# Kernel optimization log

Measured on AMD Instinct MI355X. Metric: run time of the kernel, lower is better.

Reference implementation:

```python
import jax, jax.numpy as jnp
import numpy as np

N_NODES = 50000
N_EDGES = 800000
NODE_DIM = 128
EDGE_DIM = 16
OUT_DIM = 64
HEADS = 4


def setup_inputs() -> dict:
    key = jax.random.key(0)
    ks = jax.random.split(key, 12)
    x = jax.random.normal(ks[0], (N_NODES, NODE_DIM), jnp.float32)
    edge_index = jax.random.randint(ks[1], (2, N_EDGES), 0, N_NODES)
    batch = jnp.zeros((N_NODES,), jnp.int32)
    edge_attr = jax.random.normal(ks[2], (N_EDGES, EDGE_DIM), jnp.float32)
    s = 1.0 / np.sqrt(NODE_DIM)
    W = jax.random.normal(ks[3], (NODE_DIM, HEADS * OUT_DIM), jnp.float32) * s
    att_src = jax.random.normal(ks[4], (HEADS, OUT_DIM), jnp.float32) * 0.1
    att_dst = jax.random.normal(ks[5], (HEADS, OUT_DIM), jnp.float32) * 0.1
    W_e = jax.random.normal(ks[6], (EDGE_DIM, HEADS * OUT_DIM), jnp.float32) * (1.0 / np.sqrt(EDGE_DIM))
    att_edge = jax.random.normal(ks[7], (HEADS, OUT_DIM), jnp.float32) * 0.1
    bias = jnp.zeros((OUT_DIM,), jnp.float32)
    gamma = jnp.ones((OUT_DIM,), jnp.float32)
    beta = jnp.zeros((OUT_DIM,), jnp.float32)
    return {"x": x, "edge_index": edge_index, "batch": batch, "edge_attr": edge_attr,
            "W": W, "att_src": att_src, "att_dst": att_dst, "W_e": W_e,
            "att_edge": att_edge, "bias": bias, "gamma": gamma, "beta": beta}


def reference(x, edge_index, batch, edge_attr, W, att_src, att_dst, W_e, att_edge, bias, gamma, beta):
    N = x.shape[0]
    H, C = att_src.shape
    src, dst = edge_index[0], edge_index[1]
    E = src.shape[0]

    # add self loops; self-loop edge_attr = per-node mean of incoming edge attrs (PyG fill_value='mean')
    cnt = jax.ops.segment_sum(jnp.ones((E, 1), x.dtype), dst, num_segments=N)
    loop_attr = jax.ops.segment_sum(edge_attr, dst, num_segments=N) / jnp.maximum(cnt, 1.0)
    loop_idx = jnp.arange(N, dtype=src.dtype)
    src_f = jnp.concatenate([src, loop_idx])
    dst_f = jnp.concatenate([dst, loop_idx])
    ea = jnp.concatenate([edge_attr, loop_attr], axis=0)

    h = (x @ W).reshape(N, H, C)                       # [N,H,C]
    a_src = jnp.einsum('nhc,hc->nh', h, att_src)       # [N,H]
    a_dst = jnp.einsum('nhc,hc->nh', h, att_dst)
    e_emb = (ea @ W_e).reshape(-1, H, C)               # [E',H,C]
    a_edge = jnp.einsum('ehc,hc->eh', e_emb, att_edge)

    alpha = jax.nn.leaky_relu(a_src[src_f] + a_dst[dst_f] + a_edge, 0.2)  # [E',H]
    amax = jax.ops.segment_max(alpha, dst_f, num_segments=N)
    expa = jnp.exp(alpha - amax[dst_f])
    denom = jax.ops.segment_sum(expa, dst_f, num_segments=N)
    att = expa / (denom[dst_f] + 1e-16)                # segment softmax over dst

    msg = h[src_f] * att[:, :, None]                   # [E',H,C]
    out = jax.ops.segment_sum(msg, dst_f, num_segments=N)  # [N,H,C]
    out = out.mean(axis=1) + bias                      # concat=False -> head mean

    mu = out.mean(-1, keepdims=True)
    var = out.var(-1, keepdims=True)
    out = (out - mu) / jnp.sqrt(var + 1e-5) * gamma + beta
    return jax.nn.elu(out)
```

## Files before the change

kernel.cpp:

```cpp
#include <hip/hip_runtime.h>

typedef unsigned int u32;
typedef unsigned short u16;

static constexpr int NN  = 50000;
static constexpr int EE  = 800000;
static constexpr int CAP = 64;

typedef __attribute__((ext_vector_type(8))) short bf16x8;
typedef __attribute__((ext_vector_type(4))) float f32x4;
typedef __attribute__((ext_vector_type(4))) u32   u32x4;

__device__ inline float u2f(u32 u){ union{u32 i; float f;} v; v.i=u; return v.f; }
__device__ inline float bf2f(u16 u){ return u2f(((u32)u)<<16); }
__device__ inline u16 f2bf(float f){ union{float f; u32 i;} v; v.f=f; u32 i=v.i;
    return (u16)((i + 0x7fffu + ((i>>16)&1u))>>16); }
__device__ inline u32 pk2(float a, float b){ return (u32)f2bf(a) | ((u32)f2bf(b)<<16); }
__device__ inline float lrelu(float x){ return x > 0.f ? x : 0.2f*x; }

__device__ inline u32 pkh(float a, float b){
    union{ _Float16 h[2]; u32 u; } v;
    v.h[0] = (_Float16)a; v.h[1] = (_Float16)b;
    return v.u;
}
__device__ inline float hlo(u32 u){ union{u32 u; _Float16 h[2];} v; v.u=u; return (float)v.h[0]; }
__device__ inline float hhi(u32 u){ union{u32 u; _Float16 h[2];} v; v.u=u; return (float)v.h[1]; }

__device__ inline float ld(const void* base, size_t i, int f32m){
    return f32m ? ((const float*)base)[i] : bf2f(((const u16*)base)[i]);
}

__device__ inline float wsum(float v){
    #pragma unroll
    for (int m=1;m<64;m<<=1) v += __shfl_xor(v, m, 64);
    return v;
}

#if defined(__has_builtin)
#if __has_builtin(__builtin_amdgcn_fdot2_f32_bf16)
#define HAS_DOT2 1
#endif
#endif

#ifdef HAS_DOT2
typedef __attribute__((ext_vector_type(2))) __bf16 bf16x2;
#endif

__device__ inline float dot2acc(u32 hv, u32 wv, float acc){
#ifdef HAS_DOT2
    union { u32 u; bf16x2 v; } a, b; a.u = hv; b.u = wv;
    return __builtin_amdgcn_fdot2_f32_bf16(a.v, b.v, acc, false);
#else
    acc = fmaf(u2f(hv<<16),         u2f(wv<<16),         acc);
    acc = fmaf(u2f(hv&0xffff0000u), u2f(wv&0xffff0000u), acc);
    return acc;
#endif
}

__device__ inline int detect_f32(const u16* xraw){
    int lane = threadIdx.x & 63;
    bool bad = false;
    #pragma unroll
    for (int i = 0; i < 8; ++i){
        float v = bf2f(xraw[2*(lane + i*64)]);
        if (!(fabsf(v) < 1e10f)) bad = true;
    }
    return __any(bad) ? 1 : 0;
}

__device__ inline void edge_logits(const void* ea, int e, int f32m,
                                   const float* Ml, float* A){
    float v[16];
    if (f32m){
        const f32x4* r = ((const f32x4*)ea) + (size_t)e*4;
        f32x4 a = __builtin_nontemporal_load(r);
        f32x4 b = __builtin_nontemporal_load(r+1);
        f32x4 c = __builtin_nontemporal_load(r+2);
        f32x4 d = __builtin_nontemporal_load(r+3);
        v[0]=a[0]; v[1]=a[1]; v[2]=a[2]; v[3]=a[3];
        v[4]=b[0]; v[5]=b[1]; v[6]=b[2]; v[7]=b[3];
        v[8]=c[0]; v[9]=c[1]; v[10]=c[2]; v[11]=c[3];
        v[12]=d[0]; v[13]=d[1]; v[14]=d[2]; v[15]=d[3];
    } else {
        const u32x4* r = ((const u32x4*)ea) + (size_t)e*2;
        u32x4 q0 = __builtin_nontemporal_load(r);
        u32x4 q1 = __builtin_nontemporal_load(r+1);
        v[0]=u2f(q0[0]<<16); v[1]=u2f(q0[0]&0xffff0000u);
        v[2]=u2f(q0[1]<<16); v[3]=u2f(q0[1]&0xffff0000u);
        v[4]=u2f(q0[2]<<16); v[5]=u2f(q0[2]&0xffff0000u);
        v[6]=u2f(q0[3]<<16); v[7]=u2f(q0[3]&0xffff0000u);
        v[8]=u2f(q1[0]<<16); v[9]=u2f(q1[0]&0xffff0000u);
        v[10]=u2f(q1[1]<<16); v[11]=u2f(q1[1]&0xffff0000u);
        v[12]=u2f(q1[2]<<16); v[13]=u2f(q1[2]&0xffff0000u);
        v[14]=u2f(q1[3]<<16); v[15]=u2f(q1[3]&0xffff0000u);
    }
    float a0=0,a1=0,a2=0,a3=0;
    #pragma unroll
    for (int j = 0; j < 16; ++j){
        a0 = fmaf(v[j], Ml[j*4+0], a0);
        a1 = fmaf(v[j], Ml[j*4+1], a1);
        a2 = fmaf(v[j], Ml[j*4+2], a2);
        a3 = fmaf(v[j], Ml[j*4+3], a3);
    }
    A[0]=a0; A[1]=a1; A[2]=a2; A[3]=a3;
}

__global__ __launch_bounds__(256) void k_prep(const u16* __restrict__ xraw,
                                              const void* __restrict__ W,
                                              const void* __restrict__ att_src,
                                              const void* __restrict__ att_dst,
                                              const void* __restrict__ W_e,
                                              const void* __restrict__ att_edge,
                                              int* __restrict__ flag,
                                              u16* __restrict__ Wt,
                                              float* __restrict__ Mv){
    int f32m = detect_f32(xraw);
    int b = blockIdx.x, t = threadIdx.x;
    if (b == 0){
        if (t == 0) *flag = f32m;
        if (t < 64){
            int d = t >> 2, h = t & 3;
            float s = 0.f;
            for (int c = 0; c < 64; ++c)
                s += ld(W_e, d*256 + h*64 + c, f32m) * ld(att_edge, h*64 + c, f32m);
            Mv[t] = s;
        }
    } else if (b <= 128){
        int i = (b-1)*256 + t;
        int k = i >> 8, n = i & 255;
        Wt[n*128 + k] = f2bf(ld(W, (size_t)k*256 + n, f32m));
    } else {
        int i = (b-129)*256 + t;
        int c = i >> 7, k = i & 127;
        float s = 0.f;
        if (c < 8){
            int h = c & 3;
            const void* att = (c < 4) ? att_src : att_dst;
            for (int j = 0; j < 64; ++j)
                s += ld(W, (size_t)k*256 + h*64 + j, f32m) * ld(att, h*64 + j, f32m);
        }
        Wt[(size_t)(256 + c)*128 + k] = f2bf(s);
    }
}

static constexpr int LDSROW = 136;
static constexpr int CROW   = 264;

__global__ __launch_bounds__(256) void k_gemm(const void* __restrict__ x,
                                              const u16* __restrict__ Wt,
                                              const int* __restrict__ flag,
                                              u16* __restrict__ hbuf,
                                              float* __restrict__ a_src,
                                              float* __restrict__ a_dst, int N){
    __shared__ u16 sh[64*CROW];
    int f32m = *flag;
    int t = threadIdx.x;
    int row0 = blockIdx.x*64;
    if (f32m){
        const f32x4* xg = (const f32x4*)x;
        #pragma unroll
        for (int j=0;j<8;++j){
            int idx = t + j*256;
            int r = idx >> 5, c4 = idx & 31;
            int gr = row0 + r; if (gr >= N) gr = N-1;
            f32x4 v = __builtin_nontemporal_load(&xg[(size_t)gr*32 + c4]);
            *(uint2*)&sh[r*LDSROW + c4*4] = make_uint2(pk2(v[0],v[1]), pk2(v[2],v[3]));
        }
    } else {
        const u32x4* xg = (const u32x4*)x;
        #pragma unroll
        for (int j=0;j<4;++j){
            int idx = t + j*256;
            int r = idx >> 4, c8 = idx & 15;
            int gr = row0 + r; if (gr >= N) gr = N-1;
            u32x4 v = __builtin_nontemporal_load(&xg[(size_t)gr*16 + c8]);
            *(u32x4*)&sh[r*LDSROW + c8*8] = v;
        }
    }
    __syncthreads();
    int wave = t >> 6, lane = t & 63;
    int l15 = lane & 15, quad = lane >> 4;
    int mrow = wave*16 + l15;
    bf16x8 afr[4];
    #pragma unroll
    for (int s=0;s<4;++s)
        afr[s] = *(const bf16x8*)&sh[mrow*LDSROW + s*32 + quad*8];
    __syncthreads();
    f32x4 acc[17];
    #pragma unroll
    for (int tl=0;tl<17;++tl){
        f32x4 a = {0.f,0.f,0.f,0.f};
        #pragma unroll
        for (int s=0;s<4;++s){
            bf16x8 bfr = *(const bf16x8*)&Wt[(size_t)(tl*16 + l15)*128 + s*32 + quad*8];
            a = __builtin_amdgcn_mfma_f32_16x16x32_bf16(afr[s], bfr, a, 0, 0, 0);
        }
        acc[tl] = a;
    }
    int rbase = row0 + wave*16 + quad*4;
    #pragma unroll
    for (int r=0;r<4;++r){
        int gr = rbase + r;
        if (gr < N){
            if (l15 < 4)      a_src[gr*4 + l15]     = acc[16][r];
            else if (l15 < 8) a_dst[gr*4 + (l15-4)] = acc[16][r];
        }
    }
    #pragma unroll
    for (int r=0;r<4;++r){
        int row = wave*16 + quad*4 + r;
        #pragma unroll
        for (int tl=0;tl<4;++tl){
            u32 lo = pk2(acc[tl  ][r], acc[tl+4 ][r]);
            u32 hi = pk2(acc[tl+8][r], acc[tl+12][r]);
            *(uint2*)&sh[row*CROW + (tl*16 + l15)*4] = make_uint2(lo, hi);
        }
    }
    __syncthreads();
    uint4* h4 = (uint4*)hbuf;
    #pragma unroll
    for (int j=0;j<8;++j){
        int idx = t + j*256;
        int row = idx >> 5, c16 = idx & 31;
        if (row0 + row < N){
            uint4 v = *(const uint4*)&sh[row*CROW + c16*8];
            h4[(size_t)(row0 + row)*32 + c16] = v;
        }
    }
}

__global__ __launch_bounds__(256) void k_edge(const int* __restrict__ ei,
                                              const void* __restrict__ ea,
                                              const float* __restrict__ Mv,
                                              const int* __restrict__ flag,
                                              int* __restrict__ deg,
                                              u32* __restrict__ brec, int E){
    __shared__ float Ml[64];
    if (threadIdx.x < 64) Ml[threadIdx.x] = Mv[threadIdx.x];
    __syncthreads();
    int f32m = *flag;
    int base = blockIdx.x*512 + threadIdx.x;
    #pragma unroll
    for (int j=0;j<2;++j){
        int e = base + j*256;
        if (e >= E) continue;
        int src = __builtin_nontemporal_load(&ei[e]);
        int dst = __builtin_nontemporal_load(&ei[E + e]);
        float A[4];
        edge_logits(ea, e, f32m, Ml, A);
        int slot = atomicAdd(&deg[dst], 1);
        if (slot < CAP){
            size_t i3 = ((size_t)dst*CAP + slot)*3;
            brec[i3]   = (u32)src;
            brec[i3+1] = pkh(A[0], A[1]);
            brec[i3+2] = pkh(A[2], A[3]);
        }
    }
}

__global__ __launch_bounds__(256) void k_node(const int* __restrict__ deg,
                                              const u32* __restrict__ brec,
                                              const float* __restrict__ a_src,
                                              const float* __restrict__ a_dst,
                                              const u16* __restrict__ hbuf,
                                              const void* __restrict__ bias,
                                              const void* __restrict__ gamma,
                                              const void* __restrict__ beta,
                                              const int* __restrict__ flag,
                                              void* __restrict__ out, int N){
    __shared__ uint4 lrec[4][CAP+4];
    int f32m = *flag;
    int lane = threadIdx.x & 63;
    int slot = threadIdx.x >> 6;
    int n = blockIdx.x*4 + slot;
    int dg = deg[n];
    int dc = dg < CAP ? dg : CAP;
    float4 an  = ((const float4*)a_src)[n];
    float4 adn = ((const float4*)a_dst)[n];
    bool v0 = lane < dc;
    u32 src = (u32)n;
    float w0=0.f,w1=0.f,w2=0.f,w3=0.f;
    float a0=0.f,a1=0.f,a2=0.f,a3=0.f;
    if (v0){
        const u32* rp = brec + ((size_t)n*CAP + lane)*3;
        u32 s   = rp[0];
        u32 p01 = rp[1];
        u32 p23 = rp[2];
        src = s;
        a0 = hlo(p01); a1 = hhi(p01); a2 = hlo(p23); a3 = hhi(p23);
        float4 asg = ((const float4*)a_src)[s];
        w0 = expf(lrelu(asg.x + adn.x + a0));
        w1 = expf(lrelu(asg.y + adn.y + a1));
        w2 = expf(lrelu(asg.z + adn.z + a2));
        w3 = expf(lrelu(asg.w + adn.w + a3));
    }
    float dn0 = wsum(w0), dn1 = wsum(w1), dn2 = wsum(w2), dn3 = wsum(w3);
    float invd = 1.f / (float)(dg > 1 ? dg : 1);
    float ge0 = wsum(a0)*invd, ge1 = wsum(a1)*invd;
    float ge2 = wsum(a2)*invd, ge3 = wsum(a3)*invd;
    float exS0 = expf(lrelu(an.x + adn.x + ge0));
    float exS1 = expf(lrelu(an.y + adn.y + ge1));
    float exS2 = expf(lrelu(an.z + adn.z + ge2));
    float exS3 = expf(lrelu(an.w + adn.w + ge3));
    float i0 = 0.25f/(dn0 + exS0 + 1e-16f);
    float i1 = 0.25f/(dn1 + exS1 + 1e-16f);
    float i2 = 0.25f/(dn2 + exS2 + 1e-16f);
    float i3 = 0.25f/(dn3 + exS3 + 1e-16f);
    if (v0)
        lrec[slot][lane] = make_uint4(src, pk2(w0*i0, w1*i1), pk2(w2*i2, w3*i3), 0u);
    if (lane == 0)
        lrec[slot][dc] = make_uint4((u32)n, pk2(exS0*i0, exS1*i1), pk2(exS2*i2, exS3*i3), 0u);
    else if (lane <= 3)
        lrec[slot][dc + lane] = make_uint4((u32)n, 0u, 0u, 0u);
    __syncthreads();
    int T = dc + 1;
    int iters = (T + 3) >> 2;
    int half = lane >> 5, l5 = lane & 31;
    const uint4* hb4 = (const uint4*)hbuf;
    float acc0 = 0.f, acc1 = 0.f;
    uint4 r0 = lrec[slot][half];
    uint4 r1 = lrec[slot][2 + half];
    uint4 h0 = hb4[(size_t)r0.x*32 + l5];
    uint4 h1 = hb4[(size_t)r1.x*32 + l5];
    for (int i = 1; i < iters; ++i){
        uint4 nr0 = lrec[slot][4*i + half];
        uint4 nr1 = lrec[slot][4*i + 2 + half];
        uint4 nh0 = hb4[(size_t)nr0.x*32 + l5];
        uint4 nh1 = hb4[(size_t)nr1.x*32 + l5];
        acc0 = dot2acc(h0.x, r0.y, acc0);
        acc0 = dot2acc(h0.y, r0.z, acc0);
        acc1 = dot2acc(h0.z, r0.y, acc1);
        acc1 = dot2acc(h0.w, r0.z, acc1);
        acc0 = dot2acc(h1.x, r1.y, acc0);
        acc0 = dot2acc(h1.y, r1.z, acc0);
        acc1 = dot2acc(h1.z, r1.y, acc1);
        acc1 = dot2acc(h1.w, r1.z, acc1);
        r0 = nr0; r1 = nr1; h0 = nh0; h1 = nh1;
    }
    acc0 = dot2acc(h0.x, r0.y, acc0);
    acc0 = dot2acc(h0.y, r0.z, acc0);
    acc1 = dot2acc(h0.z, r0.y, acc1);
    acc1 = dot2acc(h0.w, r0.z, acc1);
    acc0 = dot2acc(h1.x, r1.y, acc0);
    acc0 = dot2acc(h1.y, r1.z, acc0);
    acc1 = dot2acc(h1.z, r1.y, acc1);
    acc1 = dot2acc(h1.w, r1.z, acc1);
    acc0 += __shfl_xor(acc0, 32, 64);
    acc1 += __shfl_xor(acc1, 32, 64);
    float va = __shfl(acc0, lane>>1, 64);
    float vb = __shfl(acc1, lane>>1, 64);
    float o = ((lane & 1) ? vb : va) + ld(bias, lane, f32m);
    float mu = wsum(o) * (1.f/64.f);
    float d = o - mu;
    float var = wsum(d*d) * (1.f/64.f);
    float y = d * rsqrtf(var + 1e-5f) * ld(gamma, lane, f32m) + ld(beta, lane, f32m);
    y = y > 0.f ? y : expf(y) - 1.f;
    if (f32m) ((float*)out)[(size_t)n*64 + lane] = y;
    else      ((u16*)out)[(size_t)n*64 + lane] = f2bf(y);
}

extern "C" void kernel_launch(void* const* d_in, const int* in_sizes, int n_in,
                              void* d_out, int out_size, void* d_ws, size_t ws_size,
                              hipStream_t stream){
    const void* x        = d_in[0];
    const int*  ei       = (const int*)d_in[1];
    const void* ea       = d_in[3];
    const void* W        = d_in[4];
    const void* att_src  = d_in[5];
    const void* att_dst  = d_in[6];
    const void* W_e      = d_in[7];
    const void* att_edge = d_in[8];
    const void* bias     = d_in[9];
    const void* gamma    = d_in[10];
    const void* beta     = d_in[11];
    const int N = NN, E = EE;

    char* p = (char*)d_ws;
    auto alloc = [&](size_t bytes){ void* r = (void*)p; p += (bytes + 255) & ~(size_t)255; return r; };
    int*   deg   = (int*)  alloc((size_t)N*4);
    float* Mv    = (float*)alloc(64*4);
    float* a_src = (float*)alloc((size_t)N*16);
    float* a_dst = (float*)alloc((size_t)N*16);
    u32*   brec  = (u32*)  alloc((size_t)N*CAP*12);
    u16*   hbuf  = (u16*)  alloc((size_t)N*256*2);
    u16*   Wt    = (u16*)  alloc((size_t)272*128*2);
    int*   flag  = (int*)  alloc(256);

    hipMemsetAsync(deg, 0, (size_t)N*4, stream);
    k_prep<<<137, 256, 0, stream>>>((const u16*)x, W, att_src, att_dst, W_e, att_edge,
                                    flag, Wt, Mv);
    k_gemm<<<(N+63)/64, 256, 0, stream>>>(x, Wt, flag, hbuf, a_src, a_dst, N);
    k_edge<<<(E+511)/512, 256, 0, stream>>>(ei, ea, Mv, flag, deg, brec, E);
    k_node<<<N/4, 256, 0, stream>>>(deg, brec, a_src, a_dst, hbuf,
                                    bias, gamma, beta, flag, d_out, N);
}
```

Before: 289.2 us.

## Merge GEMM and edge-binning kernels into one launch; deepen gather prefetch

The node-projection GEMM and the edge logit/binning pass are independent, so they now run as two block ranges of a single kernel. This removes one launch boundary and lets edge blocks overlap with GEMM blocks. The aggregation loop in the node kernel now prefetches two iterations ahead using ping-pong register sets, which hides more of the hbuf gather latency. Bucket-record loads and output stores are marked nontemporal. In exchange, register pressure rises and the fused kernel mixes heterogeneous blocks that share one LDS allocation size.

```diff
diff --git a/kernel.cpp b/kernel.cpp
--- a/kernel.cpp
+++ b/kernel.cpp
@@ -146,114 +146,114 @@
 static constexpr int LDSROW = 136;
 static constexpr int CROW   = 264;
 
-__global__ __launch_bounds__(256) void k_gemm(const void* __restrict__ x,
-                                              const u16* __restrict__ Wt,
-                                              const int* __restrict__ flag,
-                                              u16* __restrict__ hbuf,
-                                              float* __restrict__ a_src,
-                                              float* __restrict__ a_dst, int N){
+__global__ __launch_bounds__(256) void k_gx(const void* __restrict__ x,
+                                            const u16* __restrict__ Wt,
+                                            const int* __restrict__ flag,
+                                            u16* __restrict__ hbuf,
+                                            float* __restrict__ a_src,
+                                            float* __restrict__ a_dst,
+                                            const int* __restrict__ ei,
+                                            const void* __restrict__ ea,
+                                            const float* __restrict__ Mv,
+                                            int* __restrict__ deg,
+                                            u32* __restrict__ brec,
+                                            int N, int E, int GB){
     __shared__ u16 sh[64*CROW];
+    int t = threadIdx.x;
     int f32m = *flag;
-    int t = threadIdx.x;
-    int row0 = blockIdx.x*64;
-    if (f32m){
-        const f32x4* xg = (const f32x4*)x;
+    if ((int)blockIdx.x < GB){
+        int row0 = blockIdx.x*64;
+        if (f32m){
+            const f32x4* xg = (const f32x4*)x;
+            #pragma unroll
+            for (int j=0;j<8;++j){
+                int idx = t + j*256;
+                int r = idx >> 5, c4 = idx & 31;
+                int gr = row0 + r; if (gr >= N) gr = N-1;
+                f32x4 v = __builtin_nontemporal_load(&xg[(size_t)gr*32 + c4]);
+                *(uint2*)&sh[r*LDSROW + c4*4] = make_uint2(pk2(v[0],v[1]), pk2(v[2],v[3]));
+            }
+        } else {
+            const u32x4* xg = (const u32x4*)x;
+            #pragma unroll
+            for (int j=0;j<4;++j){
+                int idx = t + j*256;
+                int r = idx >> 4, c8 = idx & 15;
+                int gr = row0 + r; if (gr >= N) gr = N-1;
+                u32x4 v = __builtin_nontemporal_load(&xg[(size_t)gr*16 + c8]);
+                *(u32x4*)&sh[r*LDSROW + c8*8] = v;
+            }
+        }
+        __syncthreads();
+        int wave = t >> 6, lane = t & 63;
+        int l15 = lane & 15, quad = lane >> 4;
+        int mrow = wave*16 + l15;
+        bf16x8 afr[4];
+        #pragma unroll
+        for (int s=0;s<4;++s)
+            afr[s] = *(const bf16x8*)&sh[mrow*LDSROW + s*32 + quad*8];
+        __syncthreads();
+        f32x4 acc[17];
+        #pragma unroll
+        for (int tl=0;tl<17;++tl){
+            f32x4 a = {0.f,0.f,0.f,0.f};
+            #pragma unroll
+            for (int s=0;s<4;++s){
+                bf16x8 bfr = *(const bf16x8*)&Wt[(size_t)(tl*16 + l15)*128 + s*32 + quad*8];
+                a = __builtin_amdgcn_mfma_f32_16x16x32_bf16(afr[s], bfr, a, 0, 0, 0);
+            }
+            acc[tl] = a;
+        }
+        int rbase = row0 + wave*16 + quad*4;
+        #pragma unroll
+        for (int r=0;r<4;++r){
+            int gr = rbase + r;
+            if (gr < N){
+                if (l15 < 4)      a_src[gr*4 + l15]     = acc[16][r];
+                else if (l15 < 8) a_dst[gr*4 + (l15-4)] = acc[16][r];
+            }
+        }
+        #pragma unroll
+        for (int r=0;r<4;++r){
+            int row = wave*16 + quad*4 + r;
+            #pragma unroll
+            for (int tl=0;tl<4;++tl){
+                u32 lo = pk2(acc[tl  ][r], acc[tl+4 ][r]);
+                u32 hi = pk2(acc[tl+8][r], acc[tl+12][r]);
+                *(uint2*)&sh[row*CROW + (tl*16 + l15)*4] = make_uint2(lo, hi);
+            }
+        }
+        __syncthreads();
+        uint4* h4 = (uint4*)hbuf;
         #pragma unroll
         for (int j=0;j<8;++j){
             int idx = t + j*256;
-            int r = idx >> 5, c4 = idx & 31;
-            int gr = row0 + r; if (gr >= N) gr = N-1;
-            f32x4 v = __builtin_nontemporal_load(&xg[(size_t)gr*32 + c4]);
-            *(uint2*)&sh[r*LDSROW + c4*4] = make_uint2(pk2(v[0],v[1]), pk2(v[2],v[3]));
+            int row = idx >> 5, c16 = idx & 31;
+            if (row0 + row < N){
+                uint4 v = *(const uint4*)&sh[row*CROW + c16*8];
+                h4[(size_t)(row0 + row)*32 + c16] = v;
+            }
         }
     } else {
-        const u32x4* xg = (const u32x4*)x;
-        #pragma unroll
-        for (int j=0;j<4;++j){
-            int idx = t + j*256;
-            int r = idx >> 4, c8 = idx & 15;
-            int gr = row0 + r; if (gr >= N) gr = N-1;
-            u32x4 v = __builtin_nontemporal_load(&xg[(size_t)gr*16 + c8]);
-            *(u32x4*)&sh[r*LDSROW + c8*8] = v;
-        }
-    }
-    __syncthreads();
-    int wave = t >> 6, lane = t & 63;
-    int l15 = lane & 15, quad = lane >> 4;
-    int mrow = wave*16 + l15;
-    bf16x8 afr[4];
-    #pragma unroll
-    for (int s=0;s<4;++s)
-        afr[s] = *(const bf16x8*)&sh[mrow*LDSROW + s*32 + quad*8];
-    __syncthreads();
-    f32x4 acc[17];
-    #pragma unroll
-    for (int tl=0;tl<17;++tl){
-        f32x4 a = {0.f,0.f,0.f,0.f};
-        #pragma unroll
-        for (int s=0;s<4;++s){
-            bf16x8 bfr = *(const bf16x8*)&Wt[(size_t)(tl*16 + l15)*128 + s*32 + quad*8];
-            a = __builtin_amdgcn_mfma_f32_16x16x32_bf16(afr[s], bfr, a, 0, 0, 0);
-        }
-        acc[tl] = a;
-    }
-    int rbase = row0 + wave*16 + quad*4;
-    #pragma unroll
-    for (int r=0;r<4;++r){
-        int gr = rbase + r;
-        if (gr < N){
-            if (l15 < 4)      a_src[gr*4 + l15]     = acc[16][r];
-            else if (l15 < 8) a_dst[gr*4 + (l15-4)] = acc[16][r];
-        }
-    }
-    #pragma unroll
-    for (int r=0;r<4;++r){
-        int row = wave*16 + quad*4 + r;
-        #pragma unroll
-        for (int tl=0;tl<4;++tl){
-            u32 lo = pk2(acc[tl  ][r], acc[tl+4 ][r]);
-            u32 hi = pk2(acc[tl+8][r], acc[tl+12][r]);
-            *(uint2*)&sh[row*CROW + (tl*16 + l15)*4] = make_uint2(lo, hi);
-        }
-    }
-    __syncthreads();
-    uint4* h4 = (uint4*)hbuf;
-    #pragma unroll
-    for (int j=0;j<8;++j){
-        int idx = t + j*256;
-        int row = idx >> 5, c16 = idx & 31;
-        if (row0 + row < N){
-            uint4 v = *(const uint4*)&sh[row*CROW + c16*8];
-            h4[(size_t)(row0 + row)*32 + c16] = v;
-        }
-    }
-}
-
-__global__ __launch_bounds__(256) void k_edge(const int* __restrict__ ei,
-                                              const void* __restrict__ ea,
-                                              const float* __restrict__ Mv,
-                                              const int* __restrict__ flag,
-                                              int* __restrict__ deg,
-                                              u32* __restrict__ brec, int E){
-    __shared__ float Ml[64];
-    if (threadIdx.x < 64) Ml[threadIdx.x] = Mv[threadIdx.x];
-    __syncthreads();
-    int f32m = *flag;
-    int base = blockIdx.x*512 + threadIdx.x;
-    #pragma unroll
-    for (int j=0;j<2;++j){
-        int e = base + j*256;
-        if (e >= E) continue;
-        int src = __builtin_nontemporal_load(&ei[e]);
-        int dst = __builtin_nontemporal_load(&ei[E + e]);
-        float A[4];
-        edge_logits(ea, e, f32m, Ml, A);
-        int slot = atomicAdd(&deg[dst], 1);
-        if (slot < CAP){
-            size_t i3 = ((size_t)dst*CAP + slot)*3;
-            brec[i3]   = (u32)src;
-            brec[i3+1] = pkh(A[0], A[1]);
-            brec[i3+2] = pkh(A[2], A[3]);
+        float* Ml = (float*)sh;
+        if (t < 64) Ml[t] = Mv[t];
+        __syncthreads();
+        int base = ((int)blockIdx.x - GB)*512 + t;
+        #pragma unroll
+        for (int j=0;j<2;++j){
+            int e = base + j*256;
+            if (e >= E) continue;
+            int src = __builtin_nontemporal_load(&ei[e]);
+            int dst = __builtin_nontemporal_load(&ei[E + e]);
+            float A[4];
+            edge_logits(ea, e, f32m, Ml, A);
+            int slot = atomicAdd(&deg[dst], 1);
+            if (slot < CAP){
+                size_t i3 = ((size_t)dst*CAP + slot)*3;
+                brec[i3]   = (u32)src;
+                brec[i3+1] = pkh(A[0], A[1]);
+                brec[i3+2] = pkh(A[2], A[3]);
+            }
         }
     }
 }
@@ -283,9 +283,9 @@
     float a0=0.f,a1=0.f,a2=0.f,a3=0.f;
     if (v0){
         const u32* rp = brec + ((size_t)n*CAP + lane)*3;
-        u32 s   = rp[0];
-        u32 p01 = rp[1];
-        u32 p23 = rp[2];
+        u32 s   = __builtin_nontemporal_load(&rp[0]);
+        u32 p01 = __builtin_nontemporal_load(&rp[1]);
+        u32 p23 = __builtin_nontemporal_load(&rp[2]);
         src = s;
         a0 = hlo(p01); a1 = hhi(p01); a2 = hlo(p23); a3 = hhi(p23);
         float4 asg = ((const float4*)a_src)[s];
@@ -318,33 +318,60 @@
     int half = lane >> 5, l5 = lane & 31;
     const uint4* hb4 = (const uint4*)hbuf;
     float acc0 = 0.f, acc1 = 0.f;
-    uint4 r0 = lrec[slot][half];
-    uint4 r1 = lrec[slot][2 + half];
-    uint4 h0 = hb4[(size_t)r0.x*32 + l5];
-    uint4 h1 = hb4[(size_t)r1.x*32 + l5];
-    for (int i = 1; i < iters; ++i){
-        uint4 nr0 = lrec[slot][4*i + half];
-        uint4 nr1 = lrec[slot][4*i + 2 + half];
-        uint4 nh0 = hb4[(size_t)nr0.x*32 + l5];
-        uint4 nh1 = hb4[(size_t)nr1.x*32 + l5];
-        acc0 = dot2acc(h0.x, r0.y, acc0);
-        acc0 = dot2acc(h0.y, r0.z, acc0);
-        acc1 = dot2acc(h0.z, r0.y, acc1);
-        acc1 = dot2acc(h0.w, r0.z, acc1);
-        acc0 = dot2acc(h1.x, r1.y, acc0);
-        acc0 = dot2acc(h1.y, r1.z, acc0);
-        acc1 = dot2acc(h1.z, r1.y, acc1);
-        acc1 = dot2acc(h1.w, r1.z, acc1);
-        r0 = nr0; r1 = nr1; h0 = nh0; h1 = nh1;
-    }
-    acc0 = dot2acc(h0.x, r0.y, acc0);
-    acc0 = dot2acc(h0.y, r0.z, acc0);
-    acc1 = dot2acc(h0.z, r0.y, acc1);
-    acc1 = dot2acc(h0.w, r0.z, acc1);
-    acc0 = dot2acc(h1.x, r1.y, acc0);
-    acc0 = dot2acc(h1.y, r1.z, acc0);
-    acc1 = dot2acc(h1.z, r1.y, acc1);
-    acc1 = dot2acc(h1.w, r1.z, acc1);
+    uint4 rA0 = lrec[slot][half];
+    uint4 rA1 = lrec[slot][2 + half];
+    uint4 hA0 = hb4[(size_t)rA0.x*32 + l5];
+    uint4 hA1 = hb4[(size_t)rA1.x*32 + l5];
+    uint4 rB0, rB1, hB0, hB1;
+    if (iters > 1){
+        rB0 = lrec[slot][4 + half];
+        rB1 = lrec[slot][6 + half];
+        hB0 = hb4[(size_t)rB0.x*32 + l5];
+        hB1 = hb4[(size_t)rB1.x*32 + l5];
+    }
+    int i = 0;
+    while (true){
+        {
+            bool pf = (i + 2 < iters);
+            uint4 nr0, nr1, nh0, nh1;
+            if (pf){
+                nr0 = lrec[slot][4*(i+2) + half];
+                nr1 = lrec[slot][4*(i+2) + 2 + half];
+                nh0 = hb4[(size_t)nr0.x*32 + l5];
+                nh1 = hb4[(size_t)nr1.x*32 + l5];
+            }
+            acc0 = dot2acc(hA0.x, rA0.y, acc0);
+            acc0 = dot2acc(hA0.y, rA0.z, acc0);
+            acc1 = dot2acc(hA0.z, rA0.y, acc1);
+            acc1 = dot2acc(hA0.w, rA0.z, acc1);
+            acc0 = dot2acc(hA1.x, rA1.y, acc0);
+            acc0 = dot2acc(hA1.y, rA1.z, acc0);
+            acc1 = dot2acc(hA1.z, rA1.y, acc1);
+            acc1 = dot2acc(hA1.w, rA1.z, acc1);
+            if (pf){ rA0=nr0; rA1=nr1; hA0=nh0; hA1=nh1; }
+            if (++i >= iters) break;
+        }
+        {
+            bool pf = (i + 2 < iters);
+            uint4 nr0, nr1, nh0, nh1;
+            if (pf){
+                nr0 = lrec[slot][4*(i+2) + half];
+                nr1 = lrec[slot][4*(i+2) + 2 + half];
+                nh0 = hb4[(size_t)nr0.x*32 + l5];
+                nh1 = hb4[(size_t)nr1.x*32 + l5];
+            }
+            acc0 = dot2acc(hB0.x, rB0.y, acc0);
+            acc0 = dot2acc(hB0.y, rB0.z, acc0);
+            acc1 = dot2acc(hB0.z, rB0.y, acc1);
+            acc1 = dot2acc(hB0.w, rB0.z, acc1);
+            acc0 = dot2acc(hB1.x, rB1.y, acc0);
+            acc0 = dot2acc(hB1.y, rB1.z, acc0);
+            acc1 = dot2acc(hB1.z, rB1.y, acc1);
+            acc1 = dot2acc(hB1.w, rB1.z, acc1);
+            if (pf){ rB0=nr0; rB1=nr1; hB0=nh0; hB1=nh1; }
+            if (++i >= iters) break;
+        }
+    }
     acc0 += __shfl_xor(acc0, 32, 64);
     acc1 += __shfl_xor(acc1, 32, 64);
     float va = __shfl(acc0, lane>>1, 64);
@@ -355,8 +382,8 @@
     float var = wsum(d*d) * (1.f/64.f);
     float y = d * rsqrtf(var + 1e-5f) * ld(gamma, lane, f32m) + ld(beta, lane, f32m);
     y = y > 0.f ? y : expf(y) - 1.f;
-    if (f32m) ((float*)out)[(size_t)n*64 + lane] = y;
-    else      ((u16*)out)[(size_t)n*64 + lane] = f2bf(y);
+    if (f32m) __builtin_nontemporal_store(y, &((float*)out)[(size_t)n*64 + lane]);
+    else      __builtin_nontemporal_store(f2bf(y), &((u16*)out)[(size_t)n*64 + lane]);
 }
 
 extern "C" void kernel_launch(void* const* d_in, const int* in_sizes, int n_in,
@@ -386,11 +413,14 @@
     u16*   Wt    = (u16*)  alloc((size_t)272*128*2);
     int*   flag  = (int*)  alloc(256);
 
+    const int GB = (N + 63)/64;
+    const int EB = (E + 511)/512;
+
     hipMemsetAsync(deg, 0, (size_t)N*4, stream);
     k_prep<<<137, 256, 0, stream>>>((const u16*)x, W, att_src, att_dst, W_e, att_edge,
                                     flag, Wt, Mv);
-    k_gemm<<<(N+63)/64, 256, 0, stream>>>(x, Wt, flag, hbuf, a_src, a_dst, N);
-    k_edge<<<(E+511)/512, 256, 0, stream>>>(ei, ea, Mv, flag, deg, brec, E);
+    k_gx<<<GB + EB, 256, 0, stream>>>(x, Wt, flag, hbuf, a_src, a_dst,
+                                      ei, ea, Mv, deg, brec, N, E, GB);
     k_node<<<N/4, 256, 0, stream>>>(deg, brec, a_src, a_dst, hbuf,
                                     bias, gamma, beta, flag, d_out, N);
 }
```

Result: faster. 277.5 us (-4.1%).
